# Kernel tuning notes

Measured on AMD Instinct MI355X. Metric: run time of the kernel, lower is better.

The kernel has to match this reference:

```python
import jax, jax.numpy as jnp
import numpy as np

H, W, C, E = 6, 40, 512, 128  # hardcoded in module


def setup_inputs() -> dict:
    key = jax.random.key(0)
    ks = jax.random.split(key, 9)
    nB = 512
    inp = {
        "prev_hidden": jax.random.normal(ks[0], (nB, C), jnp.float32),
        "conv_feats": jax.random.normal(ks[1], (nB, C, H, W), jnp.float32),
        "conv_feats_origin": jax.random.normal(ks[2], (nB, C, H, W), jnp.float32),
        "cur_embeddings": jax.random.normal(ks[3], (nB, E), jnp.float32),
        # params
        "score_w": jax.random.normal(ks[4], (C,), jnp.float32) * (1.0 / np.sqrt(C)),
        "w_ih": jax.random.normal(ks[5], (3 * C, C + E), jnp.float32) * (1.0 / np.sqrt(C)),
        "w_hh": jax.random.normal(ks[6], (3 * C, C), jnp.float32) * (1.0 / np.sqrt(C)),
        "b_ih": jax.random.normal(ks[7], (3 * C,), jnp.float32) * 0.01,
        "b_hh": jax.random.normal(ks[8], (3 * C,), jnp.float32) * 0.01,
    }
    return inp


def gru_cell(x, h, w_ih, w_hh, b_ih, b_hh):
    # PyTorch GRUCell semantics
    gi = x @ w_ih.T + b_ih            # [B, 3C]
    gh = h @ w_hh.T + b_hh            # [B, 3C]
    i_r, i_z, i_n = jnp.split(gi, 3, axis=1)
    h_r, h_z, h_n = jnp.split(gh, 3, axis=1)
    r = jax.nn.sigmoid(i_r + h_r)
    z = jax.nn.sigmoid(i_z + h_z)
    n = jnp.tanh(i_n + r * h_n)
    return (1.0 - z) * n + z * h


def reference(prev_hidden, conv_feats, conv_feats_origin, cur_embeddings,
              score_w, w_ih, w_hh, b_ih, b_hh):
    nB = prev_hidden.shape[0]
    cf = conv_feats.reshape(nB, C, H * W)          # [B, C, HW]
    cfo = conv_feats_origin.reshape(nB, C, H * W)  # [B, C, HW]
    # additive attention score: tanh(feat + h) . score_w
    e = jnp.tanh(cf + prev_hidden[:, :, None])      # [B, C, HW]
    emition = jnp.einsum('bch,c->bh', e, score_w)   # [B, HW]
    alpha = jax.nn.softmax(emition, axis=1)         # softmax over HW positions
    context = jnp.einsum('bch,bh->bc', cfo, alpha)  # [B, C]
    x = jnp.concatenate([context, cur_embeddings], axis=1)  # [B, C+E]
    cur_hidden = gru_cell(x, prev_hidden, w_ih, w_hh, b_ih, b_hh)
    return cur_hidden, alpha.T  # alpha returned as [HW, B] like the original
```

## Files before the change

### kernel.cpp

```cpp
#include <hip/hip_runtime.h>
#include <hip/hip_bf16.h>

#define B   512
#define C   512
#define HW  240
#define HW4 60
#define E   128
#define XD  640
#define G3  1536

typedef short  s8v  __attribute__((ext_vector_type(8)));
typedef float  f4v  __attribute__((ext_vector_type(4)));

__device__ __forceinline__ float fast_tanh(float x) {
    float ex = __expf(2.0f * x);
    return (ex - 1.0f) * __builtin_amdgcn_rcpf(ex + 1.0f);
}
__device__ __forceinline__ float fast_sigmoid(float x) {
    return __builtin_amdgcn_rcpf(1.0f + __expf(-x));
}
__device__ __forceinline__ unsigned short f2bf(float x) {
    return __builtin_bit_cast(unsigned short, __float2bfloat16(x));
}
__device__ __forceinline__ s8v pack8(float4 a, float4 b) {
    s8v o;
    o[0] = (short)f2bf(a.x); o[1] = (short)f2bf(a.y);
    o[2] = (short)f2bf(a.z); o[3] = (short)f2bf(a.w);
    o[4] = (short)f2bf(b.x); o[5] = (short)f2bf(b.y);
    o[6] = (short)f2bf(b.z); o[7] = (short)f2bf(b.w);
    return o;
}

__global__ __launch_bounds__(512) void attn_kernel(
    const float* __restrict__ prev_hidden,
    const float* __restrict__ conv_feats,
    const float* __restrict__ cfo,
    const float* __restrict__ cur_emb,
    const float* __restrict__ score_w,
    float* __restrict__ alpha_out,
    unsigned short* __restrict__ x_bf16)
{
    const int b    = blockIdx.x;
    const int t    = threadIdx.x;
    const int w    = t >> 6;
    const int lane = t & 63;

    __shared__ float ph2_s[C];
    __shared__ float msw_s[C];
    __shared__ f4v   red[8][HW4];
    __shared__ f4v   af4[HW4];

    ph2_s[t] = 2.0f * prev_hidden[(size_t)b * C + t];
    msw_s[t] = -2.0f * score_w[t];
    if (t < E) x_bf16[(size_t)b * XD + C + t] = f2bf(cur_emb[(size_t)b * E + t]);
    __syncthreads();

    {
        const int g = w;
        const int i = lane;
        f4v acc = {0.f, 0.f, 0.f, 0.f};
        if (i < HW4) {
            const float4* cf4 = (const float4*)conv_feats
                              + (size_t)(b * C + g * 64) * HW4 + i;
            #pragma unroll 8
            for (int j = 0; j < 64; ++j) {
                float4 v  = cf4[(size_t)j * HW4];
                float ph2 = ph2_s[g * 64 + j];
                float msw = msw_s[g * 64 + j];
                acc[0] += msw * __builtin_amdgcn_rcpf(__expf(fmaf(v.x, 2.0f, ph2)) + 1.0f);
                acc[1] += msw * __builtin_amdgcn_rcpf(__expf(fmaf(v.y, 2.0f, ph2)) + 1.0f);
                acc[2] += msw * __builtin_amdgcn_rcpf(__expf(fmaf(v.z, 2.0f, ph2)) + 1.0f);
                acc[3] += msw * __builtin_amdgcn_rcpf(__expf(fmaf(v.w, 2.0f, ph2)) + 1.0f);
            }
            red[g][i] = acc;
        }
    }
    __syncthreads();

    if (w == 0) {
        const bool act = lane < HW4;
        f4v e4 = {0.f, 0.f, 0.f, 0.f};
        if (act) {
            #pragma unroll
            for (int g = 0; g < 8; ++g) {
                f4v r = red[g][lane];
                e4[0] += r[0]; e4[1] += r[1]; e4[2] += r[2]; e4[3] += r[3];
            }
        }
        float mx = act ? fmaxf(fmaxf(e4[0], e4[1]), fmaxf(e4[2], e4[3])) : -1e30f;
        #pragma unroll
        for (int off = 32; off >= 1; off >>= 1) mx = fmaxf(mx, __shfl_xor(mx, off));

        f4v p4;
        p4[0] = act ? __expf(e4[0] - mx) : 0.f;
        p4[1] = act ? __expf(e4[1] - mx) : 0.f;
        p4[2] = act ? __expf(e4[2] - mx) : 0.f;
        p4[3] = act ? __expf(e4[3] - mx) : 0.f;
        float s = p4[0] + p4[1] + p4[2] + p4[3];
        #pragma unroll
        for (int off = 32; off >= 1; off >>= 1) s += __shfl_xor(s, off);
        float inv = __builtin_amdgcn_rcpf(s);

        if (act) {
            f4v a;
            a[0] = p4[0] * inv; a[1] = p4[1] * inv;
            a[2] = p4[2] * inv; a[3] = p4[3] * inv;
            af4[lane] = a;
            float* ao = alpha_out + b;
            ao[(size_t)(4 * lane + 0) * B] = a[0];
            ao[(size_t)(4 * lane + 1) * B] = a[1];
            ao[(size_t)(4 * lane + 2) * B] = a[2];
            ao[(size_t)(4 * lane + 3) * B] = a[3];
        }
    }
    __syncthreads();

    const int r0 = (w << 4) + (lane >> 2);
    const int q  = lane & 3;
    #pragma unroll
    for (int p = 0; p < 4; ++p) {
        const int r = p * 128 + r0;
        const float4* row = (const float4*)cfo + (size_t)(b * C + r) * HW4;
        float acc = 0.f;
        #pragma unroll
        for (int k = 0; k < 15; ++k) {
            float4 v = row[q + 4 * k];
            f4v   av = af4[q + 4 * k];
            acc += v.x * av[0] + v.y * av[1] + v.z * av[2] + v.w * av[3];
        }
        acc += __shfl_xor(acc, 1);
        acc += __shfl_xor(acc, 2);
        if (q == 0) x_bf16[(size_t)b * XD + r] = f2bf(acc);
    }
}

__global__ __launch_bounds__(256) void gemm_kernel(
    const unsigned short* __restrict__ x,
    const float* __restrict__ hprev,
    const float* __restrict__ wih,
    const float* __restrict__ whh,
    const float* __restrict__ b_ih, const float* __restrict__ b_hh,
    float* __restrict__ gi, float* __restrict__ gh)
{
    const int z = blockIdx.z;
    const float* Wmat = z ? whh : wih;
    const float* bias = z ? b_hh : b_ih;
    float* out = z ? gh : gi;
    const int K = z ? C : XD;

    const int b0 = blockIdx.x * 64;
    const int j0 = blockIdx.y * 64;

    __shared__ alignas(16) unsigned short As[64][72];
    __shared__ alignas(16) unsigned short Ws[64][72];

    const int t = threadIdx.x, lane = t & 63, w = t >> 6;
    const int wm = w & 1, wn = w >> 1;
    const int r = t >> 2, col0 = (t & 3) * 16;
    const int q = lane >> 4, mm = lane & 15;

    f4v z4 = {0.f, 0.f, 0.f, 0.f};
    f4v acc[2][2] = {{z4, z4}, {z4, z4}};

    for (int k0 = 0; k0 < K; k0 += 64) {
        s8v a0, a1, w0, w1;
        if (z) {
            const float4* pa = (const float4*)&hprev[(size_t)(b0 + r) * C + k0 + col0];
            float4 f0 = pa[0], f1 = pa[1], f2 = pa[2], f3 = pa[3];
            a0 = pack8(f0, f1); a1 = pack8(f2, f3);
        } else {
            const unsigned short* pa = &x[(size_t)(b0 + r) * XD + k0 + col0];
            a0 = *(const s8v*)pa; a1 = *(const s8v*)(pa + 8);
        }
        {
            const float4* pw = (const float4*)&Wmat[(size_t)(j0 + r) * K + k0 + col0];
            float4 f0 = pw[0], f1 = pw[1], f2 = pw[2], f3 = pw[3];
            w0 = pack8(f0, f1); w1 = pack8(f2, f3);
        }
        __syncthreads();
        *(s8v*)&As[r][col0]     = a0;
        *(s8v*)&As[r][col0 + 8] = a1;
        *(s8v*)&Ws[r][col0]     = w0;
        *(s8v*)&Ws[r][col0 + 8] = w1;
        __syncthreads();

        #pragma unroll
        for (int kk = 0; kk < 2; ++kk) {
            s8v av0 = *(const s8v*)&As[wm * 32 + mm][kk * 32 + q * 8];
            s8v av1 = *(const s8v*)&As[wm * 32 + 16 + mm][kk * 32 + q * 8];
            s8v wv0 = *(const s8v*)&Ws[wn * 32 + mm][kk * 32 + q * 8];
            s8v wv1 = *(const s8v*)&Ws[wn * 32 + 16 + mm][kk * 32 + q * 8];
            acc[0][0] = __builtin_amdgcn_mfma_f32_16x16x32_bf16(av0, wv0, acc[0][0], 0, 0, 0);
            acc[0][1] = __builtin_amdgcn_mfma_f32_16x16x32_bf16(av0, wv1, acc[0][1], 0, 0, 0);
            acc[1][0] = __builtin_amdgcn_mfma_f32_16x16x32_bf16(av1, wv0, acc[1][0], 0, 0, 0);
            acc[1][1] = __builtin_amdgcn_mfma_f32_16x16x32_bf16(av1, wv1, acc[1][1], 0, 0, 0);
        }
    }

    #pragma unroll
    for (int mi = 0; mi < 2; ++mi)
        #pragma unroll
        for (int ni = 0; ni < 2; ++ni) {
            int jj = j0 + wn * 32 + ni * 16 + mm;
            float bv = bias[jj];
            #pragma unroll
            for (int rg = 0; rg < 4; ++rg) {
                int bi = b0 + wm * 32 + mi * 16 + q * 4 + rg;
                out[(size_t)bi * G3 + jj] = acc[mi][ni][rg] + bv;
            }
        }
}

__global__ void gates_kernel(const float* __restrict__ gi,
                             const float* __restrict__ gh,
                             const float* __restrict__ hprev,
                             float* __restrict__ out)
{
    int idx = blockIdx.x * blockDim.x + threadIdx.x;
    if (idx >= B * C) return;
    int b = idx >> 9;
    int c = idx & 511;
    const float* gib = gi + (size_t)b * G3;
    const float* ghb = gh + (size_t)b * G3;
    float r  = fast_sigmoid(gib[c] + ghb[c]);
    float zz = fast_sigmoid(gib[c + C] + ghb[c + C]);
    float n  = fast_tanh(gib[c + 2 * C] + r * ghb[c + 2 * C]);
    out[idx] = (1.f - zz) * n + zz * hprev[idx];
}

extern "C" void kernel_launch(void* const* d_in, const int* in_sizes, int n_in,
                              void* d_out, int out_size, void* d_ws, size_t ws_size,
                              hipStream_t stream)
{
    const float* prev_hidden = (const float*)d_in[0];
    const float* conv_feats  = (const float*)d_in[1];
    const float* cfo         = (const float*)d_in[2];
    const float* emb         = (const float*)d_in[3];
    const float* score_w     = (const float*)d_in[4];
    const float* w_ih        = (const float*)d_in[5];
    const float* w_hh        = (const float*)d_in[6];
    const float* b_ih        = (const float*)d_in[7];
    const float* b_hh        = (const float*)d_in[8];

    float* out       = (float*)d_out;
    float* alpha_out = out + B * C;

    char* ws = (char*)d_ws;
    float* gi              = (float*)(ws);
    float* gh              = (float*)(ws + 3145728);
    unsigned short* x_bf16 = (unsigned short*)(ws + 6291456);

    attn_kernel<<<dim3(B), 512, 0, stream>>>(prev_hidden, conv_feats, cfo, emb,
                                             score_w, alpha_out, x_bf16);
    gemm_kernel<<<dim3(8, 24, 2), 256, 0, stream>>>(x_bf16, prev_hidden, w_ih, w_hh,
                                                    b_ih, b_hh, gi, gh);
    gates_kernel<<<(B * C + 255) / 256, 256, 0, stream>>>(gi, gh, prev_hidden, out);
}
```

Baseline: 515.8 us.

## Double attention block to 1024 threads with prefetched row loads

The attention kernel now launches 1024 threads per batch row, so 16 waves each handle 32 channels instead of 8 waves handling 64. The score loop is unrolled by two with explicit prefetch of the next two float4 rows, and the context pass splits its rows across twice as many waves. The transposed alpha store is spread over 240 threads instead of being done by one wave. The aim is more memory-level parallelism on the bandwidth-bound reads of conv_feats and conv_feats_origin, at the cost of a larger reduction buffer and higher register pressure under the new launch bounds.

```diff
diff --git a/kernel.cpp b/kernel.cpp
--- a/kernel.cpp
+++ b/kernel.cpp
@@ -31,7 +31,7 @@
     return o;
 }
 
-__global__ __launch_bounds__(512) void attn_kernel(
+__global__ __launch_bounds__(1024, 8) void attn_kernel(
     const float* __restrict__ prev_hidden,
     const float* __restrict__ conv_feats,
     const float* __restrict__ cfo,
@@ -47,34 +47,44 @@
 
     __shared__ float ph2_s[C];
     __shared__ float msw_s[C];
-    __shared__ f4v   red[8][HW4];
+    __shared__ f4v   red[16][HW4];
     __shared__ f4v   af4[HW4];
 
-    ph2_s[t] = 2.0f * prev_hidden[(size_t)b * C + t];
-    msw_s[t] = -2.0f * score_w[t];
+    if (t < C) {
+        ph2_s[t] = 2.0f * prev_hidden[(size_t)b * C + t];
+        msw_s[t] = -2.0f * score_w[t];
+    }
     if (t < E) x_bf16[(size_t)b * XD + C + t] = f2bf(cur_emb[(size_t)b * E + t]);
     __syncthreads();
 
-    {
-        const int g = w;
-        const int i = lane;
+#define ROWACC(vv, jj) {                                                        \
+        float ph2 = ph2_s[w * 32 + (jj)];                                       \
+        float msw = msw_s[w * 32 + (jj)];                                       \
+        acc[0] += msw * __builtin_amdgcn_rcpf(__expf(fmaf(vv.x, 2.0f, ph2)) + 1.0f); \
+        acc[1] += msw * __builtin_amdgcn_rcpf(__expf(fmaf(vv.y, 2.0f, ph2)) + 1.0f); \
+        acc[2] += msw * __builtin_amdgcn_rcpf(__expf(fmaf(vv.z, 2.0f, ph2)) + 1.0f); \
+        acc[3] += msw * __builtin_amdgcn_rcpf(__expf(fmaf(vv.w, 2.0f, ph2)) + 1.0f); \
+    }
+    if (lane < HW4) {
+        const float4* cf4 = (const float4*)conv_feats
+                          + (size_t)(b * C + w * 32) * HW4 + lane;
         f4v acc = {0.f, 0.f, 0.f, 0.f};
-        if (i < HW4) {
-            const float4* cf4 = (const float4*)conv_feats
-                              + (size_t)(b * C + g * 64) * HW4 + i;
-            #pragma unroll 8
-            for (int j = 0; j < 64; ++j) {
-                float4 v  = cf4[(size_t)j * HW4];
-                float ph2 = ph2_s[g * 64 + j];
-                float msw = msw_s[g * 64 + j];
-                acc[0] += msw * __builtin_amdgcn_rcpf(__expf(fmaf(v.x, 2.0f, ph2)) + 1.0f);
-                acc[1] += msw * __builtin_amdgcn_rcpf(__expf(fmaf(v.y, 2.0f, ph2)) + 1.0f);
-                acc[2] += msw * __builtin_amdgcn_rcpf(__expf(fmaf(v.z, 2.0f, ph2)) + 1.0f);
-                acc[3] += msw * __builtin_amdgcn_rcpf(__expf(fmaf(v.w, 2.0f, ph2)) + 1.0f);
+        float4 v0 = cf4[0];
+        float4 v1 = cf4[HW4];
+        #pragma unroll
+        for (int j = 0; j < 32; j += 2) {
+            float4 n0, n1;
+            if (j + 2 < 32) {
+                n0 = cf4[(size_t)(j + 2) * HW4];
+                n1 = cf4[(size_t)(j + 3) * HW4];
             }
-            red[g][i] = acc;
-        }
-    }
+            ROWACC(v0, j);
+            ROWACC(v1, j + 1);
+            if (j + 2 < 32) { v0 = n0; v1 = n1; }
+        }
+        red[w][lane] = acc;
+    }
+#undef ROWACC
     __syncthreads();
 
     if (w == 0) {
@@ -82,7 +92,7 @@
         f4v e4 = {0.f, 0.f, 0.f, 0.f};
         if (act) {
             #pragma unroll
-            for (int g = 0; g < 8; ++g) {
+            for (int g = 0; g < 16; ++g) {
                 f4v r = red[g][lane];
                 e4[0] += r[0]; e4[1] += r[1]; e4[2] += r[2]; e4[3] += r[3];
             }
@@ -106,20 +116,17 @@
             a[0] = p4[0] * inv; a[1] = p4[1] * inv;
             a[2] = p4[2] * inv; a[3] = p4[3] * inv;
             af4[lane] = a;
-            float* ao = alpha_out + b;
-            ao[(size_t)(4 * lane + 0) * B] = a[0];
-            ao[(size_t)(4 * lane + 1) * B] = a[1];
-            ao[(size_t)(4 * lane + 2) * B] = a[2];
-            ao[(size_t)(4 * lane + 3) * B] = a[3];
         }
     }
     __syncthreads();
+
+    if (t < HW) alpha_out[(size_t)t * B + b] = ((const float*)af4)[t];
 
     const int r0 = (w << 4) + (lane >> 2);
     const int q  = lane & 3;
     #pragma unroll
-    for (int p = 0; p < 4; ++p) {
-        const int r = p * 128 + r0;
+    for (int p = 0; p < 2; ++p) {
+        const int r = (p << 8) | r0;
         const float4* row = (const float4*)cfo + (size_t)(b * C + r) * HW4;
         float acc = 0.f;
         #pragma unroll
@@ -250,8 +257,8 @@
     float* gh              = (float*)(ws + 3145728);
     unsigned short* x_bf16 = (unsigned short*)(ws + 6291456);
 
-    attn_kernel<<<dim3(B), 512, 0, stream>>>(prev_hidden, conv_feats, cfo, emb,
-                                             score_w, alpha_out, x_bf16);
+    attn_kernel<<<dim3(B), 1024, 0, stream>>>(prev_hidden, conv_feats, cfo, emb,
+                                              score_w, alpha_out, x_bf16);
     gemm_kernel<<<dim3(8, 24, 2), 256, 0, stream>>>(x_bf16, prev_hidden, w_ih, w_hh,
                                                     b_ih, b_hh, gi, gh);
     gates_kernel<<<(B * C + 255) / 256, 256, 0, stream>>>(gi, gh, prev_hidden, out);
```

New measurement: 523.5 us. About the same (+1.5%).
